# Kernel optimization log

Measured on AMD Instinct MI355X. Metric: run time of the kernel, lower is better.

Reference implementation:

```python
import jax, jax.numpy as jnp
import numpy as np

N = 16384
F_IN = 256
F_OUT = 256


def setup_inputs() -> dict:
    key = jax.random.key(0)
    k1, k2, k3 = jax.random.split(key, 3)
    x = jax.random.normal(k1, (N, F_IN), dtype=jnp.float32)
    # dense 0/1 adjacency (original masks with adj[j] == 1)
    adj = jax.random.randint(k2, (N, N), 0, 2, dtype=jnp.int32)
    # glorot-uniform init for weight [2F_in, F_out]
    stdv = np.sqrt(6.0 / (2 * F_IN + F_OUT)).astype(np.float32)
    weight = jax.random.uniform(k3, (2 * F_IN, F_OUT), dtype=jnp.float32,
                                minval=-stdv, maxval=stdv)
    bias = jnp.zeros((F_OUT,), dtype=jnp.float32)
    return {"x": x, "adj": adj, "weight": weight, "bias": bias}


def reference(x, adj, weight, bias):
    # Mean over neighbors (adj row == 1): segment-mean expressed as a
    # normalized dense matmul -- equivalent to the per-row boolean-mask mean.
    a = adj.astype(x.dtype)                      # [N, N]
    deg = jnp.sum(a, axis=1, keepdims=True)      # [N, 1]
    x1 = (a @ x) / deg                           # [N, F] neighbor mean
    n_x = jnp.concatenate([x1, x], axis=1)       # [N, 2F]
    return n_x @ weight + bias                   # [N, F_out]
```

## Files before the change

### kernel.cpp

```cpp
#include <hip/hip_runtime.h>
#include <hip/hip_bf16.h>
#include <stdint.h>


typedef short bf16x8 __attribute__((ext_vector_type(8)));
typedef float f32x4  __attribute__((ext_vector_type(4)));

__device__ __forceinline__ uint32_t pack_bf16_rne(float lo, float hi) {
    uint32_t ul = __float_as_uint(lo);
    uint32_t uh = __float_as_uint(hi);
    ul = (ul + 0x7fffu + ((ul >> 16) & 1u)) >> 16;
    uh = (uh + 0x7fffu + ((uh >> 16) & 1u)) >> 16;
    return ul | (uh << 16);
}

__device__ __forceinline__ void gload_lds16(const void* g, void* l) {
    __builtin_amdgcn_global_load_lds(
        (__attribute__((address_space(1))) void*)g,
        (__attribute__((address_space(3))) void*)l, 16, 0, 0);
}

__global__ __launch_bounds__(256) void k_transpose_w(const float* __restrict__ w,
                                                     uint16_t* __restrict__ wt) {
    int idx = blockIdx.x * 256 + threadIdx.x;
    int n = idx >> 8;
    int k = idx & 255;
    int row = (n < 256) ? k : (256 + k);
    int col = (n < 256) ? n : (n - 256);
    uint32_t u = __float_as_uint(w[row * 256 + col]);
    u = (u + 0x7fffu + ((u >> 16) & 1u)) >> 16;
    wt[idx] = (uint16_t)u;
}

__global__ __launch_bounds__(256) void k_small_gemm(const float* __restrict__ x,
                                                    const uint16_t* __restrict__ wt,
                                                    const float* __restrict__ bias,
                                                    uint16_t* __restrict__ yT,
                                                    float* __restrict__ z) {
    __shared__ uint16_t As[128 * 32];
    __shared__ uint16_t Bs[128 * 32];

    const int t  = threadIdx.x;
    const int ct = blockIdx.x;
    const int rt = blockIdx.y;
    const int m0 = rt * 128;
    const int n0 = ct * 128;

    const int lane = t & 63, w = t >> 6;
    const int wr = w >> 1, wc = w & 1;
    const int l15 = lane & 15, quad = lane >> 4;

    f32x4 acc[4][4] = {};

    float4 a_reg[4];
    uint4  b_reg[2];

#pragma unroll
    for (int i = 0; i < 4; ++i) {
        int f4 = t + 256 * i, row = f4 >> 3, c4 = f4 & 7;
        a_reg[i] = *(const float4*)(x + (m0 + row) * 256 + c4 * 4);
    }
#pragma unroll
    for (int i = 0; i < 2; ++i) {
        int u4 = t + 256 * i, n_l = u4 >> 2, part = u4 & 3;
        b_reg[i] = *(const uint4*)(wt + (n0 + n_l) * 256 + part * 8);
    }

    for (int kk = 0; kk < 8; ++kk) {
        __syncthreads();
#pragma unroll
        for (int i = 0; i < 4; ++i) {
            int f4 = t + 256 * i, row = f4 >> 3, c4 = f4 & 7;
            uint2 p;
            p.x = pack_bf16_rne(a_reg[i].x, a_reg[i].y);
            p.y = pack_bf16_rne(a_reg[i].z, a_reg[i].w);
            *(uint2*)(As + row * 32 + c4 * 4) = p;
        }
#pragma unroll
        for (int i = 0; i < 2; ++i) {
            int u4 = t + 256 * i, n_l = u4 >> 2, part = u4 & 3;
            *(uint4*)(Bs + n_l * 32 + part * 8) = b_reg[i];
        }
        if (kk < 7) {
            int k0 = (kk + 1) * 32;
#pragma unroll
            for (int i = 0; i < 4; ++i) {
                int f4 = t + 256 * i, row = f4 >> 3, c4 = f4 & 7;
                a_reg[i] = *(const float4*)(x + (m0 + row) * 256 + k0 + c4 * 4);
            }
#pragma unroll
            for (int i = 0; i < 2; ++i) {
                int u4 = t + 256 * i, n_l = u4 >> 2, part = u4 & 3;
                b_reg[i] = *(const uint4*)(wt + (n0 + n_l) * 256 + k0 + part * 8);
            }
        }
        __syncthreads();

        bf16x8 a_frag[4], b_frag[4];
#pragma unroll
        for (int fr = 0; fr < 4; ++fr)
            a_frag[fr] = *(const bf16x8*)(As + (wr * 64 + fr * 16 + l15) * 32 + quad * 8);
#pragma unroll
        for (int fc = 0; fc < 4; ++fc)
            b_frag[fc] = *(const bf16x8*)(Bs + (wc * 64 + fc * 16 + l15) * 32 + quad * 8);
#pragma unroll
        for (int fr = 0; fr < 4; ++fr)
#pragma unroll
            for (int fc = 0; fc < 4; ++fc)
                acc[fr][fc] = __builtin_amdgcn_mfma_f32_16x16x32_bf16(
                    a_frag[fr], b_frag[fc], acc[fr][fc], 0, 0, 0);
    }

    if (ct < 2) {
#pragma unroll
        for (int fr = 0; fr < 4; ++fr) {
            int m_base = m0 + wr * 64 + fr * 16 + quad * 4;
#pragma unroll
            for (int fc = 0; fc < 4; ++fc) {
                int n_g = n0 + wc * 64 + fc * 16 + l15;
                uint2 pp;
                pp.x = pack_bf16_rne(acc[fr][fc][0], acc[fr][fc][1]);
                pp.y = pack_bf16_rne(acc[fr][fc][2], acc[fr][fc][3]);
                *(uint2*)(yT + (size_t)n_g * 16384 + m_base) = pp;
            }
        }
    } else {
#pragma unroll
        for (int fr = 0; fr < 4; ++fr) {
            int m_base = m0 + wr * 64 + fr * 16 + quad * 4;
#pragma unroll
            for (int fc = 0; fc < 4; ++fc) {
                int n_g = (n0 - 256) + wc * 64 + fc * 16 + l15;
                float bv = bias[n_g];
#pragma unroll
                for (int r = 0; r < 4; ++r)
                    z[(size_t)(m_base + r) * 256 + n_g] = acc[fr][fc][r] + bv;
            }
        }
    }
}

#define A_STRIDE 40
#define A_SZ (64 * A_STRIDE)
#define B_SZ (256 * 32)
#define KITER 256
__global__ __launch_bounds__(512, 4) void k_big_gemm(const int* __restrict__ adj,
                                                     const uint16_t* __restrict__ yT,
                                                     float* __restrict__ part,
                                                     int* __restrict__ degw) {
    __shared__ uint16_t As_f[2 * A_SZ];
    __shared__ uint16_t Bs_f[2 * B_SZ];

    const int t = threadIdx.x;
    const int m0 = blockIdx.x * 64;
    const int ky = blockIdx.y;
    const int kbase = ky * 8192;
    const int lane = t & 63, w = t >> 6;
    const int wr = w >> 2, wc = w & 3;
    const int l15 = lane & 15, quad = lane >> 4;

    f32x4 acc[2][4] = {};

    const int a_n = t >> 3, a_c4 = t & 7;
    const int4* pa4 = (const int4*)(adj + (size_t)(m0 + a_n) * 16384 + kbase) + a_c4;
    const int a_lds = a_n * A_STRIDE + a_c4 * 4;

    const uint16_t* pbg[2];
    int b_ldsbase[2];
#pragma unroll
    for (int i = 0; i < 2; ++i) {
        int base = (w * 2 + i) * 64;
        int s = base + lane;
        int bn = s >> 2;
        int bc = (s & 3) ^ ((bn >> 1) & 3);
        pbg[i] = yT + (size_t)bn * 16384 + kbase + bc * 8;
        b_ldsbase[i] = base * 8;
    }

#pragma unroll
    for (int i = 0; i < 2; ++i) {
        gload_lds16(pbg[i], &Bs_f[b_ldsbase[i]]);
        pbg[i] += 32;
    }
    int4 a = pa4[0]; pa4 += 8;
    int degp = a.x + a.y + a.z + a.w;
    {
        uint2 pv;
        pv.x = (uint32_t)(a.x | (a.y << 16)) * 0x3F80u;
        pv.y = (uint32_t)(a.z | (a.w << 16)) * 0x3F80u;
        *(uint2*)&As_f[a_lds] = pv;
    }
    __syncthreads();

    for (int kk = 0; kk < KITER; ++kk) {
        const int p = kk & 1;
        int4 an;
        if (kk < KITER - 1) {
            an = pa4[0]; pa4 += 8;
#pragma unroll
            for (int i = 0; i < 2; ++i) {
                gload_lds16(pbg[i], &Bs_f[(1 - p) * B_SZ + b_ldsbase[i]]);
                pbg[i] += 32;
            }
        }

        const uint16_t* Ar = As_f + p * A_SZ;
        const uint16_t* Br = Bs_f + p * B_SZ;
        bf16x8 af[2], bfr[4];
#pragma unroll
        for (int fr = 0; fr < 2; ++fr) {
            int row = wr * 32 + fr * 16 + l15;
            af[fr] = *(const bf16x8*)(Ar + row * A_STRIDE + quad * 8);
        }
#pragma unroll
        for (int fc = 0; fc < 4; ++fc) {
            int n = wc * 64 + fc * 16 + l15;
            int cs = quad ^ ((n >> 1) & 3);
            bfr[fc] = *(const bf16x8*)(Br + n * 32 + cs * 8);
        }
#pragma unroll
        for (int fr = 0; fr < 2; ++fr)
#pragma unroll
            for (int fc = 0; fc < 4; ++fc)
                acc[fr][fc] = __builtin_amdgcn_mfma_f32_16x16x32_bf16(
                    af[fr], bfr[fc], acc[fr][fc], 0, 0, 0);

        if (kk < KITER - 1) {
            degp += an.x + an.y + an.z + an.w;
            uint2 pv;
            pv.x = (uint32_t)(an.x | (an.y << 16)) * 0x3F80u;
            pv.y = (uint32_t)(an.z | (an.w << 16)) * 0x3F80u;
            *(uint2*)&As_f[(1 - p) * A_SZ + a_lds] = pv;
        }
        __syncthreads();
    }

    degp += __shfl_down(degp, 4);
    degp += __shfl_down(degp, 2);
    degp += __shfl_down(degp, 1);
    if ((t & 7) == 0) degw[ky * 16384 + m0 + a_n] = degp;

    float* pc = part + (size_t)ky * 16384 * 256;
#pragma unroll
    for (int fr = 0; fr < 2; ++fr) {
#pragma unroll
        for (int r = 0; r < 4; ++r) {
            int m_l = wr * 32 + fr * 16 + quad * 4 + r;
            size_t mrow = (size_t)(m0 + m_l) * 256;
#pragma unroll
            for (int fc = 0; fc < 4; ++fc) {
                int n_g = wc * 64 + fc * 16 + l15;
                pc[mrow + n_g] = acc[fr][fc][r];
            }
        }
    }
}

__global__ __launch_bounds__(256) void k_reduce(const float* __restrict__ part,
                                                const int* __restrict__ degw,
                                                const float* __restrict__ z,
                                                float* __restrict__ out) {
    int i4 = blockIdx.x * 256 + threadIdx.x;
    int m = i4 >> 6;
    float4 p0 = ((const float4*)part)[i4];
    float4 p1 = ((const float4*)part)[i4 + 16384 * 64];
    float4 zz = ((const float4*)z)[i4];
    float inv = 1.0f / (float)(degw[m] + degw[16384 + m]);
    float4 o;
    o.x = (p0.x + p1.x) * inv + zz.x;
    o.y = (p0.y + p1.y) * inv + zz.y;
    o.z = (p0.z + p1.z) * inv + zz.z;
    o.w = (p0.w + p1.w) * inv + zz.w;
    ((float4*)out)[i4] = o;
}

extern "C" void kernel_launch(void* const* d_in, const int* in_sizes, int n_in,
                              void* d_out, int out_size, void* d_ws, size_t ws_size,
                              hipStream_t stream) {
    const float* x      = (const float*)d_in[0];
    const int*   adj    = (const int*)d_in[1];
    const float* weight = (const float*)d_in[2];
    const float* bias   = (const float*)d_in[3];
    float* out = (float*)d_out;

    uint16_t* wt   = (uint16_t*)d_ws;
    uint16_t* yT   = (uint16_t*)((char*)d_ws + 262144);
    float*    z    = (float*)((char*)d_ws + 262144 + 8388608);
    float*    partb= (float*)((char*)d_ws + 262144 + 8388608 + 16777216);
    int*      degw = (int*)((char*)d_ws + 262144 + 8388608 + 16777216 + 33554432);

    k_transpose_w<<<512, 256, 0, stream>>>(weight, wt);
    k_small_gemm<<<dim3(4, 128), 256, 0, stream>>>(x, wt, bias, yT, z);
    k_big_gemm<<<dim3(256, 2), 512, 0, stream>>>(adj, yT, partb, degw);
    k_reduce<<<4096, 256, 0, stream>>>(partb, degw, z, out);
}
```

Measured before the change: 1.525 ms.

## Load MFMA fragments directly from global memory, dropping LDS staging and barriers

The big adjacency GEMM no longer stages adj and yT tiles through double-buffered shared memory. Each wave now loads its own A and B fragments straight into registers with a one-step register prefetch, and converts the 0/1 ints to bf16 in registers. This removes the LDS writes and reads and the per-iteration __syncthreads. In exchange, the four column-waves each re-read the same adj rows and pairs of waves re-read the same yT rows, so the savings depend on L1/L2 absorbing that duplicated traffic. Degree counting moves to the wc==0 waves and is reduced with cross-quad shuffles.

```diff
diff --git a/kernel.cpp b/kernel.cpp
--- a/kernel.cpp
+++ b/kernel.cpp
@@ -12,12 +12,6 @@
     ul = (ul + 0x7fffu + ((ul >> 16) & 1u)) >> 16;
     uh = (uh + 0x7fffu + ((uh >> 16) & 1u)) >> 16;
     return ul | (uh << 16);
-}
-
-__device__ __forceinline__ void gload_lds16(const void* g, void* l) {
-    __builtin_amdgcn_global_load_lds(
-        (__attribute__((address_space(1))) void*)g,
-        (__attribute__((address_space(3))) void*)l, 16, 0, 0);
 }
 
 __global__ __launch_bounds__(256) void k_transpose_w(const float* __restrict__ w,
@@ -140,17 +134,11 @@
     }
 }
 
-#define A_STRIDE 40
-#define A_SZ (64 * A_STRIDE)
-#define B_SZ (256 * 32)
 #define KITER 256
 __global__ __launch_bounds__(512, 4) void k_big_gemm(const int* __restrict__ adj,
                                                      const uint16_t* __restrict__ yT,
                                                      float* __restrict__ part,
                                                      int* __restrict__ degw) {
-    __shared__ uint16_t As_f[2 * A_SZ];
-    __shared__ uint16_t Bs_f[2 * B_SZ];
-
     const int t = threadIdx.x;
     const int m0 = blockIdx.x * 64;
     const int ky = blockIdx.y;
@@ -161,84 +149,74 @@
 
     f32x4 acc[2][4] = {};
 
-    const int a_n = t >> 3, a_c4 = t & 7;
-    const int4* pa4 = (const int4*)(adj + (size_t)(m0 + a_n) * 16384 + kbase) + a_c4;
-    const int a_lds = a_n * A_STRIDE + a_c4 * 4;
-
-    const uint16_t* pbg[2];
-    int b_ldsbase[2];
-#pragma unroll
-    for (int i = 0; i < 2; ++i) {
-        int base = (w * 2 + i) * 64;
-        int s = base + lane;
-        int bn = s >> 2;
-        int bc = (s & 3) ^ ((bn >> 1) & 3);
-        pbg[i] = yT + (size_t)bn * 16384 + kbase + bc * 8;
-        b_ldsbase[i] = base * 8;
-    }
-
-#pragma unroll
-    for (int i = 0; i < 2; ++i) {
-        gload_lds16(pbg[i], &Bs_f[b_ldsbase[i]]);
-        pbg[i] += 32;
-    }
-    int4 a = pa4[0]; pa4 += 8;
-    int degp = a.x + a.y + a.z + a.w;
-    {
-        uint2 pv;
-        pv.x = (uint32_t)(a.x | (a.y << 16)) * 0x3F80u;
-        pv.y = (uint32_t)(a.z | (a.w << 16)) * 0x3F80u;
-        *(uint2*)&As_f[a_lds] = pv;
-    }
-    __syncthreads();
+    const int* pa0 = adj + (size_t)(m0 + wr * 32 + l15) * 16384 + kbase + quad * 8;
+    const int* pa1 = pa0 + (size_t)16 * 16384;
+    const uint16_t* pb0 = yT + (size_t)(wc * 64 +  0 + l15) * 16384 + kbase + quad * 8;
+    const uint16_t* pb1 = pb0 + (size_t)16 * 16384;
+    const uint16_t* pb2 = pb0 + (size_t)32 * 16384;
+    const uint16_t* pb3 = pb0 + (size_t)48 * 16384;
+
+    int4 n0lo = *(const int4*)pa0, n0hi = *(const int4*)(pa0 + 4);
+    int4 n1lo = *(const int4*)pa1, n1hi = *(const int4*)(pa1 + 4);
+    uint4 nb0 = *(const uint4*)pb0, nb1 = *(const uint4*)pb1;
+    uint4 nb2 = *(const uint4*)pb2, nb3 = *(const uint4*)pb3;
+    pa0 += 32; pa1 += 32; pb0 += 32; pb1 += 32; pb2 += 32; pb3 += 32;
+
+    int deg0 = 0, deg1 = 0;
+    const bool is_deg = (wc == 0);
 
     for (int kk = 0; kk < KITER; ++kk) {
-        const int p = kk & 1;
-        int4 an;
+        int4 c0lo = n0lo, c0hi = n0hi, c1lo = n1lo, c1hi = n1hi;
+        uint4 cb0 = nb0, cb1 = nb1, cb2 = nb2, cb3 = nb3;
+
         if (kk < KITER - 1) {
-            an = pa4[0]; pa4 += 8;
-#pragma unroll
-            for (int i = 0; i < 2; ++i) {
-                gload_lds16(pbg[i], &Bs_f[(1 - p) * B_SZ + b_ldsbase[i]]);
-                pbg[i] += 32;
-            }
-        }
-
-        const uint16_t* Ar = As_f + p * A_SZ;
-        const uint16_t* Br = Bs_f + p * B_SZ;
-        bf16x8 af[2], bfr[4];
-#pragma unroll
-        for (int fr = 0; fr < 2; ++fr) {
-            int row = wr * 32 + fr * 16 + l15;
-            af[fr] = *(const bf16x8*)(Ar + row * A_STRIDE + quad * 8);
-        }
-#pragma unroll
-        for (int fc = 0; fc < 4; ++fc) {
-            int n = wc * 64 + fc * 16 + l15;
-            int cs = quad ^ ((n >> 1) & 3);
-            bfr[fc] = *(const bf16x8*)(Br + n * 32 + cs * 8);
-        }
-#pragma unroll
-        for (int fr = 0; fr < 2; ++fr)
-#pragma unroll
-            for (int fc = 0; fc < 4; ++fc)
-                acc[fr][fc] = __builtin_amdgcn_mfma_f32_16x16x32_bf16(
-                    af[fr], bfr[fc], acc[fr][fc], 0, 0, 0);
-
-        if (kk < KITER - 1) {
-            degp += an.x + an.y + an.z + an.w;
-            uint2 pv;
-            pv.x = (uint32_t)(an.x | (an.y << 16)) * 0x3F80u;
-            pv.y = (uint32_t)(an.z | (an.w << 16)) * 0x3F80u;
-            *(uint2*)&As_f[(1 - p) * A_SZ + a_lds] = pv;
-        }
-        __syncthreads();
-    }
-
-    degp += __shfl_down(degp, 4);
-    degp += __shfl_down(degp, 2);
-    degp += __shfl_down(degp, 1);
-    if ((t & 7) == 0) degw[ky * 16384 + m0 + a_n] = degp;
+            n0lo = *(const int4*)pa0; n0hi = *(const int4*)(pa0 + 4);
+            n1lo = *(const int4*)pa1; n1hi = *(const int4*)(pa1 + 4);
+            nb0 = *(const uint4*)pb0; nb1 = *(const uint4*)pb1;
+            nb2 = *(const uint4*)pb2; nb3 = *(const uint4*)pb3;
+            pa0 += 32; pa1 += 32; pb0 += 32; pb1 += 32; pb2 += 32; pb3 += 32;
+        }
+
+        uint4 u0, u1;
+        u0.x = (uint32_t)(c0lo.x | (c0lo.y << 16)) * 0x3F80u;
+        u0.y = (uint32_t)(c0lo.z | (c0lo.w << 16)) * 0x3F80u;
+        u0.z = (uint32_t)(c0hi.x | (c0hi.y << 16)) * 0x3F80u;
+        u0.w = (uint32_t)(c0hi.z | (c0hi.w << 16)) * 0x3F80u;
+        u1.x = (uint32_t)(c1lo.x | (c1lo.y << 16)) * 0x3F80u;
+        u1.y = (uint32_t)(c1lo.z | (c1lo.w << 16)) * 0x3F80u;
+        u1.z = (uint32_t)(c1hi.x | (c1hi.y << 16)) * 0x3F80u;
+        u1.w = (uint32_t)(c1hi.z | (c1hi.w << 16)) * 0x3F80u;
+
+        if (is_deg) {
+            deg0 += c0lo.x + c0lo.y + c0lo.z + c0lo.w + c0hi.x + c0hi.y + c0hi.z + c0hi.w;
+            deg1 += c1lo.x + c1lo.y + c1lo.z + c1lo.w + c1hi.x + c1hi.y + c1hi.z + c1hi.w;
+        }
+
+        bf16x8 af0 = *(bf16x8*)&u0;
+        bf16x8 af1 = *(bf16x8*)&u1;
+        bf16x8 bf0 = *(bf16x8*)&cb0;
+        bf16x8 bf1 = *(bf16x8*)&cb1;
+        bf16x8 bf2 = *(bf16x8*)&cb2;
+        bf16x8 bf3 = *(bf16x8*)&cb3;
+
+        acc[0][0] = __builtin_amdgcn_mfma_f32_16x16x32_bf16(af0, bf0, acc[0][0], 0, 0, 0);
+        acc[0][1] = __builtin_amdgcn_mfma_f32_16x16x32_bf16(af0, bf1, acc[0][1], 0, 0, 0);
+        acc[0][2] = __builtin_amdgcn_mfma_f32_16x16x32_bf16(af0, bf2, acc[0][2], 0, 0, 0);
+        acc[0][3] = __builtin_amdgcn_mfma_f32_16x16x32_bf16(af0, bf3, acc[0][3], 0, 0, 0);
+        acc[1][0] = __builtin_amdgcn_mfma_f32_16x16x32_bf16(af1, bf0, acc[1][0], 0, 0, 0);
+        acc[1][1] = __builtin_amdgcn_mfma_f32_16x16x32_bf16(af1, bf1, acc[1][1], 0, 0, 0);
+        acc[1][2] = __builtin_amdgcn_mfma_f32_16x16x32_bf16(af1, bf2, acc[1][2], 0, 0, 0);
+        acc[1][3] = __builtin_amdgcn_mfma_f32_16x16x32_bf16(af1, bf3, acc[1][3], 0, 0, 0);
+    }
+
+    if (is_deg) {
+        deg0 += __shfl_down(deg0, 16); deg0 += __shfl_down(deg0, 32);
+        deg1 += __shfl_down(deg1, 16); deg1 += __shfl_down(deg1, 32);
+        if (lane < 16) {
+            degw[ky * 16384 + m0 + wr * 32 + l15]      = deg0;
+            degw[ky * 16384 + m0 + wr * 32 + 16 + l15] = deg1;
+        }
+    }
 
     float* pc = part + (size_t)ky * 16384 * 256;
 #pragma unroll
```

New measurement: 2.101 ms. 37.8% more time.
